# Kernel optimization log

Hardware: AMD Instinct MI355X
Metric: run time of the kernel (lower is better)

The kernel has to match this reference:

```python
import jax, jax.numpy as jnp
import numpy as np

B, T, N, F_IN = 2, 24, 20000, 32
E, H, OUT, K = 320000, 128, 1, 2


def setup_inputs() -> dict:
    key = jax.random.key(0)
    ks = jax.random.split(key, 20)
    x_seq = jax.random.normal(ks[0], (B, T, N, F_IN), dtype=jnp.float32)
    edge_index = jax.random.randint(ks[1], (2, E), 0, N, dtype=jnp.int64)
    edge_weight = jax.random.uniform(ks[2], (E,), dtype=jnp.float32)

    def cheb_w(k, din):
        s = 1.0 / np.sqrt(din)
        return jax.random.uniform(k, (K, din, H), dtype=jnp.float32, minval=-s, maxval=s)

    inp = {
        "x_seq": x_seq, "edge_index": edge_index, "edge_weight": edge_weight,
        "Wxz": cheb_w(ks[3], F_IN), "bxz": jnp.zeros((H,), jnp.float32),
        "Whz": cheb_w(ks[4], H),    "bhz": jnp.zeros((H,), jnp.float32),
        "Wxr": cheb_w(ks[5], F_IN), "bxr": jnp.zeros((H,), jnp.float32),
        "Whr": cheb_w(ks[6], H),    "bhr": jnp.zeros((H,), jnp.float32),
        "Wxh": cheb_w(ks[7], F_IN), "bxh": jnp.zeros((H,), jnp.float32),
        "Whh": cheb_w(ks[8], H),    "bhh": jnp.zeros((H,), jnp.float32),
        "Wl": jax.random.normal(ks[9], (H, OUT), dtype=jnp.float32) * (1.0 / np.sqrt(H)),
        "bl": jnp.zeros((OUT,), jnp.float32),
    }
    return inp


def reference(x_seq, edge_index, edge_weight,
              Wxz, bxz, Whz, bhz, Wxr, bxr, Whr, bhr,
              Wxh, bxh, Whh, bhh, Wl, bl):
    src, dst = edge_index[0], edge_index[1]
    n = x_seq.shape[2]
    # sym-normalized scaled Laplacian with lambda_max=2: Ltilde = -D^{-1/2} A D^{-1/2}
    deg = jnp.zeros((n,), x_seq.dtype).at[src].add(edge_weight)
    dinv = jnp.where(deg > 0, jax.lax.rsqrt(jnp.where(deg > 0, deg, 1.0)), 0.0)
    norm = (-dinv[src] * edge_weight * dinv[dst])  # [E]

    def prop(x):  # x: [B,N,C] -> Ltilde @ x
        msg = x[:, src, :] * norm[None, :, None]          # [B,E,C]
        return jnp.zeros_like(x).at[:, dst, :].add(msg)

    def cheb(x, W, b):  # ChebConv K=2: T0 = x, T1 = Ltilde x
        return x @ W[0] + prop(x) @ W[1] + b

    def step(h, x_t):  # h,x_t: [B,N,*]
        z = jax.nn.sigmoid(cheb(x_t, Wxz, bxz) + cheb(h, Whz, bhz))
        r = jax.nn.sigmoid(cheb(x_t, Wxr, bxr) + cheb(h, Whr, bhr))
        h_tilde = jnp.tanh(cheb(x_t, Wxh, bxh) + cheb(h * r, Whh, bhh))
        h_new = z * h + (1.0 - z) * h_tilde
        return h_new, None

    h0 = jnp.zeros((x_seq.shape[0], n, Whz.shape[2]), x_seq.dtype)
    h_final, _ = jax.lax.scan(step, h0, jnp.swapaxes(x_seq, 0, 1))  # scan over T
    return jax.nn.relu(h_final) @ Wl + bl  # [B,N,OUT]
```

## Files before the change

kernel.cpp:

```cpp
#include <hip/hip_runtime.h>
#include <math.h>

#define NN 20000
#define NE 320000
#define BB 2
#define TT 24
#define FI 32
#define HH 128

__global__ void k_detect(const int* __restrict__ ei, int* __restrict__ flag) {
    int t = threadIdx.x;
    int nz = 0;
    for (int i = 0; i < 4; ++i) nz |= (ei[2 * (t + 64 * i) + 1] != 0);
    unsigned long long m = __ballot(nz);
    if (t == 0) flag[0] = (m != 0ull) ? 0 : 1;
}

__device__ __forceinline__ int eidx(const int* __restrict__ ei, int i, int f64) {
    return f64 ? ei[2 * i] : ei[i];
}


__global__ void k_deg_count(const int* __restrict__ ei, const float* __restrict__ w,
                            float* __restrict__ deg, int* __restrict__ counts,
                            const int* __restrict__ flag) {
    int e = blockIdx.x * blockDim.x + threadIdx.x;
    if (e >= NE) return;
    int f64 = flag[0];
    int s = eidx(ei, e, f64);
    int d = eidx(ei, NE + e, f64);
    atomicAdd(&deg[s], w[e]);
    atomicAdd(&counts[d], 1);
}

__global__ void k_dinv(const float* __restrict__ deg, float* __restrict__ dinv) {
    int n = blockIdx.x * blockDim.x + threadIdx.x;
    if (n >= NN) return;
    float d = deg[n];
    dinv[n] = d > 0.f ? rsqrtf(d) : 0.f;
}

__global__ void k_norm(const int* __restrict__ ei, const float* __restrict__ w,
                       const float* __restrict__ dinv, float* __restrict__ normv,
                       const int* __restrict__ flag) {
    int e = blockIdx.x * blockDim.x + threadIdx.x;
    if (e >= NE) return;
    int f64 = flag[0];
    normv[e] = -dinv[eidx(ei, e, f64)] * w[e] * dinv[eidx(ei, NE + e, f64)];
}

__global__ void k_scan(const int* __restrict__ counts, int* __restrict__ rowptr) {
    __shared__ int sums[1024];
    int t = threadIdx.x;
    const int CH = (NN + 1023) / 1024;
    int start = t * CH;
    int s = 0;
    for (int i = 0; i < CH; ++i) {
        int idx = start + i;
        if (idx < NN) s += counts[idx];
    }
    sums[t] = s;
    __syncthreads();
    for (int off = 1; off < 1024; off *= 2) {
        int v = (t >= off) ? sums[t - off] : 0;
        __syncthreads();
        sums[t] += v;
        __syncthreads();
    }
    int run = (t > 0) ? sums[t - 1] : 0;
    for (int i = 0; i < CH; ++i) {
        int idx = start + i;
        if (idx < NN) { rowptr[idx] = run; run += counts[idx]; }
    }
    if (t == 1023) rowptr[NN] = sums[1023];
}

__global__ void k_copy_int(const int* __restrict__ src, int* __restrict__ dst, int n) {
    int i = blockIdx.x * blockDim.x + threadIdx.x;
    if (i < n) dst[i] = src[i];
}

__global__ void k_fill(const int* __restrict__ ei, const float* __restrict__ normv,
                       int* __restrict__ cursor, int* __restrict__ col, float* __restrict__ val,
                       const int* __restrict__ flag) {
    int e = blockIdx.x * blockDim.x + threadIdx.x;
    if (e >= NE) return;
    int f64 = flag[0];
    int d = eidx(ei, NE + e, f64);
    int p = atomicAdd(&cursor[d], 1);
    col[p] = eidx(ei, e, f64);
    val[p] = normv[e];
}


__global__ void k_prop_x(const float* __restrict__ x_seq, int t0,
                         const int* __restrict__ rowptr, const int* __restrict__ col,
                         const float* __restrict__ val, float* __restrict__ px) {
    int n = blockIdx.x;
    int tl = blockIdx.y;
    int t = t0 + tl;
    int f = threadIdx.x & 31;
    int b = threadIdx.x >> 5;
    int beg = rowptr[n], end = rowptr[n + 1];
    const float* xb = x_seq + ((long)(b * TT + t) * NN) * FI;
    float acc = 0.f;
    for (int j = beg; j < end; ++j)
        acc += val[j] * xb[(long)col[j] * FI + f];
    px[(((long)tl * BB + b) * NN + n) * FI + f] = acc;
}

__global__ void k_prop_h(const float* __restrict__ hin,
                         const int* __restrict__ rowptr, const int* __restrict__ col,
                         const float* __restrict__ val, float* __restrict__ out) {
    int n = blockIdx.x;
    int b = blockIdx.y;
    int f = threadIdx.x;
    int beg = rowptr[n], end = rowptr[n + 1];
    const float* hb = hin + (long)b * NN * HH;
    float acc = 0.f;
    for (int j = beg; j < end; ++j)
        acc += val[j] * hb[(long)col[j] * HH + f];
    out[((long)b * NN + n) * HH + f] = acc;
}

template<int KX1, int KX2, int KH1, int KH2, int EPI>
__global__ __launch_bounds__(128)
void k_gemm(const float* __restrict__ A1, long a1_bstride,
            const float* __restrict__ A2,
            const float* __restrict__ A3,
            const float* __restrict__ A4,
            const float* __restrict__ Wx0, const float* __restrict__ Wh0,
            const float* __restrict__ bx0, const float* __restrict__ bh0,
            const float* __restrict__ Wx1, const float* __restrict__ Wh1,
            const float* __restrict__ bx1, const float* __restrict__ bh1,
            const float* __restrict__ hcur,
            const float* __restrict__ zin,
            float* __restrict__ out0,
            float* __restrict__ out1) {
    constexpr int BM = 64, BN = 64, BK = 16, NW = 128;
    constexpr int C1 = KX1, C2 = KX1 + KX2, C3 = C2 + KH1, KT = C3 + KH2;
    constexpr int NCH = KT / BK;
    static_assert(NCH * BK == KT, "K must be a multiple of BK");
    __shared__ float As[BK][BM + 4];
    __shared__ float Ws[BK][BN];
    const int tid = threadIdx.x;
    const int tx = tid & 15, ty = tid >> 4;
    const int row0 = blockIdx.x * BM;
    const int gate   = (EPI == 1) ? (int)(blockIdx.y >> 1) : 0;
    const int colblk = (EPI == 1) ? (int)(blockIdx.y & 1) : (int)blockIdx.y;
    const int col0 = colblk * BN;

    const float* Wx = Wx0; const float* Wh = Wh0;
    const float* bx = bx0; const float* bh = bh0;
    if (EPI == 1 && gate) { Wx = Wx1; Wh = Wh1; bx = bx1; bh = bh1; }

    const int rA  = tid >> 1;
    const int kqA = (tid & 1) * 8;
    const int rowg = row0 + rA;
    const int b = rowg / NN;
    const int n = rowg - b * NN;
    const long offA1 = (long)b * a1_bstride + (long)n * KX1 + kqA;
    const long offA2 = (long)rowg * KX2 + kqA;
    const long offA3 = (long)rowg * KH1 + kqA;
    const long offA4 = (long)rowg * KH2 + kqA;
    const int kWr = ty;
    const int cW  = tx * 4;

    float4 aS0, aS1, wS0, wS1;
    auto LOADA = [&](int ch) {
        const int kbase = ch * BK;
        const float* s;
        if (kbase < C1)      s = A1 + offA1 + kbase;
        else if (kbase < C2) s = A2 + offA2 + (kbase - C1);
        else if (kbase < C3) s = A3 + offA3 + (kbase - C2);
        else                 s = A4 + offA4 + (kbase - C3);
        aS0 = *(const float4*)s;
        aS1 = *(const float4*)(s + 4);
    };
    auto LOADW = [&](int ch) {
        const int kbase = ch * BK;
        const int kg0 = kbase + kWr, kg1 = kbase + kWr + 8;
        const float* s0 = (kg0 < C2) ? (Wx + (long)kg0 * NW) : (Wh + (long)(kg0 - C2) * NW);
        const float* s1 = (kg1 < C2) ? (Wx + (long)kg1 * NW) : (Wh + (long)(kg1 - C2) * NW);
        wS0 = *(const float4*)(s0 + col0 + cW);
        wS1 = *(const float4*)(s1 + col0 + cW);
    };

    float acc[8][4];
#pragma unroll
    for (int i = 0; i < 8; ++i)
#pragma unroll
        for (int j = 0; j < 4; ++j) acc[i][j] = 0.f;

    LOADA(0); LOADW(0);
    for (int ch = 0; ch < NCH; ++ch) {
        __syncthreads();
        As[kqA + 0][rA] = aS0.x;
        As[kqA + 1][rA] = aS0.y;
        As[kqA + 2][rA] = aS0.z;
        As[kqA + 3][rA] = aS0.w;
        As[kqA + 4][rA] = aS1.x;
        As[kqA + 5][rA] = aS1.y;
        As[kqA + 6][rA] = aS1.z;
        As[kqA + 7][rA] = aS1.w;
        *(float4*)&Ws[kWr][cW]     = wS0;
        *(float4*)&Ws[kWr + 8][cW] = wS1;
        __syncthreads();
        if (ch + 1 < NCH) { LOADA(ch + 1); LOADW(ch + 1); }
#pragma unroll
        for (int kk = 0; kk < BK; ++kk) {
            float4 a0 = *(const float4*)&As[kk][ty << 2];
            float4 a1 = *(const float4*)&As[kk][32 + (ty << 2)];
            float4 w  = *(const float4*)&Ws[kk][tx << 2];
            float a_[8] = {a0.x, a0.y, a0.z, a0.w, a1.x, a1.y, a1.z, a1.w};
            float w_[4] = {w.x, w.y, w.z, w.w};
#pragma unroll
            for (int i = 0; i < 8; ++i)
#pragma unroll
                for (int j = 0; j < 4; ++j)
                    acc[i][j] += a_[i] * w_[j];
        }
    }

    const int cg = col0 + (tx << 2);
    float4 bsum;
    bsum.x = bx[cg + 0] + bh[cg + 0];
    bsum.y = bx[cg + 1] + bh[cg + 1];
    bsum.z = bx[cg + 2] + bh[cg + 2];
    bsum.w = bx[cg + 3] + bh[cg + 3];
#pragma unroll
    for (int i = 0; i < 8; ++i) {
        const int row = row0 + ((i < 4) ? ((ty << 2) + i) : (32 + (ty << 2) + (i - 4)));
        const long o = (long)row * 128 + cg;
        float4 v;
        v.x = acc[i][0] + bsum.x;
        v.y = acc[i][1] + bsum.y;
        v.z = acc[i][2] + bsum.z;
        v.w = acc[i][3] + bsum.w;
        if (EPI == 1) {
            float4 s;
            s.x = 1.f / (1.f + expf(-v.x));
            s.y = 1.f / (1.f + expf(-v.y));
            s.z = 1.f / (1.f + expf(-v.z));
            s.w = 1.f / (1.f + expf(-v.w));
            if (gate == 0) {
                *(float4*)&out0[o] = s;
            } else {
                float4 hc = *(const float4*)&hcur[o];
                s.x *= hc.x; s.y *= hc.y; s.z *= hc.z; s.w *= hc.w;
                *(float4*)&out1[o] = s;
            }
        } else {
            float4 hc = *(const float4*)&hcur[o];
            float4 z  = *(const float4*)&zin[o];
            float4 r;
            r.x = z.x * hc.x + (1.f - z.x) * tanhf(v.x);
            r.y = z.y * hc.y + (1.f - z.y) * tanhf(v.y);
            r.z = z.z * hc.z + (1.f - z.z) * tanhf(v.z);
            r.w = z.w * hc.w + (1.f - z.w) * tanhf(v.w);
            *(float4*)&out0[o] = r;
        }
    }
}

__global__ void k_out(const float* __restrict__ h, const float* __restrict__ Wl,
                      const float* __restrict__ bl, float* __restrict__ out) {
    int row = blockIdx.x;
    int lane = threadIdx.x;
    const float* hr = h + (long)row * HH;
    float a = fmaxf(hr[lane], 0.f) * Wl[lane] + fmaxf(hr[64 + lane], 0.f) * Wl[64 + lane];
#pragma unroll
    for (int off = 32; off > 0; off >>= 1) a += __shfl_down(a, off);
    if (lane == 0) out[row] = a + bl[0];
}

extern "C" void kernel_launch(void* const* d_in, const int* in_sizes, int n_in,
                              void* d_out, int out_size, void* d_ws, size_t ws_size,
                              hipStream_t stream) {
    const float* x_seq = (const float*)d_in[0];
    const int*   ei    = (const int*)d_in[1];
    const float* ew    = (const float*)d_in[2];
    const float* Wxz = (const float*)d_in[3],  *bxz = (const float*)d_in[4];
    const float* Whz = (const float*)d_in[5],  *bhz = (const float*)d_in[6];
    const float* Wxr = (const float*)d_in[7],  *bxr = (const float*)d_in[8];
    const float* Whr = (const float*)d_in[9],  *bhr = (const float*)d_in[10];
    const float* Wxh = (const float*)d_in[11], *bxh = (const float*)d_in[12];
    const float* Whh = (const float*)d_in[13], *bhh = (const float*)d_in[14];
    const float* Wl  = (const float*)d_in[15], *bl  = (const float*)d_in[16];
    float* out = (float*)d_out;

    char* p = (char*)d_ws;
    auto alloc = [&](size_t bytes) -> char* {
        char* r = p;
        p += (bytes + 255) & ~(size_t)255;
        return r;
    };
    const long RB = (long)BB * NN;

    int*   dflag  = (int*)alloc(4);
    float* deg    = (float*)alloc(NN * 4);
    float* dinv   = (float*)alloc(NN * 4);
    float* normv  = (float*)alloc(NE * 4);
    int*   counts = (int*)alloc(NN * 4);
    int*   rowptr = (int*)alloc((NN + 1) * 4);
    int*   cursor = (int*)alloc(NN * 4);
    int*   ccol   = (int*)alloc(NE * 4);
    float* cval   = (float*)alloc(NE * 4);
    float* hbuf   = (float*)alloc(RB * HH * 4);
    float* ph     = (float*)alloc(RB * HH * 4);
    float* zbuf   = (float*)alloc(RB * HH * 4);
    float* hrbuf  = (float*)alloc(RB * HH * 4);

    size_t used = (size_t)(p - (char*)d_ws);
    bool batched = (ws_size > used) && ((ws_size - used) >= (size_t)TT * RB * FI * 4 + 256);
    float* px = (float*)alloc(batched ? (size_t)TT * RB * FI * 4 : (size_t)RB * FI * 4);

    hipMemsetAsync(deg, 0, NN * 4, stream);
    hipMemsetAsync(counts, 0, NN * 4, stream);
    k_detect<<<1, 64, 0, stream>>>(ei, dflag);
    k_deg_count<<<(NE + 255) / 256, 256, 0, stream>>>(ei, ew, deg, counts, dflag);
    k_dinv<<<(NN + 255) / 256, 256, 0, stream>>>(deg, dinv);
    k_norm<<<(NE + 255) / 256, 256, 0, stream>>>(ei, ew, dinv, normv, dflag);
    k_scan<<<1, 1024, 0, stream>>>(counts, rowptr);
    k_copy_int<<<(NN + 255) / 256, 256, 0, stream>>>(rowptr, cursor, NN);
    k_fill<<<(NE + 255) / 256, 256, 0, stream>>>(ei, normv, cursor, ccol, cval, dflag);

    hipMemsetAsync(hbuf, 0, RB * HH * 4, stream);

    if (batched)
        k_prop_x<<<dim3(NN, TT), 64, 0, stream>>>(x_seq, 0, rowptr, ccol, cval, px);

    const long xbstride = (long)TT * NN * FI;
    dim3 gZR(625, 4), gH(625, 2);
    for (int t = 0; t < TT; ++t) {
        const float* xt  = x_seq + (long)t * NN * FI;
        const float* pxt = batched ? (px + (long)t * RB * FI) : px;
        if (!batched)
            k_prop_x<<<dim3(NN, 1), 64, 0, stream>>>(x_seq, t, rowptr, ccol, cval, px);

        k_prop_h<<<dim3(NN, BB), HH, 0, stream>>>(hbuf, rowptr, ccol, cval, ph);
        k_gemm<FI, FI, HH, HH, 1><<<gZR, 128, 0, stream>>>(
            xt, xbstride, pxt, hbuf, ph,
            Wxz, Whz, bxz, bhz, Wxr, Whr, bxr, bhr,
            hbuf, nullptr, zbuf, hrbuf);
        k_prop_h<<<dim3(NN, BB), HH, 0, stream>>>(hrbuf, rowptr, ccol, cval, ph);
        k_gemm<FI, FI, HH, HH, 2><<<gH, 128, 0, stream>>>(
            xt, xbstride, pxt, hrbuf, ph,
            Wxh, Whh, bxh, bhh, nullptr, nullptr, nullptr, nullptr,
            hbuf, zbuf, hbuf, nullptr);
    }

    k_out<<<RB, 64, 0, stream>>>(hbuf, Wl, bl, out);
}
```

Before: 8.089 ms.

## Replace FP32 SIMT GEMM with split-bf16 MFMA and vectorize sparse propagation

```diff
diff --git a/kernel.cpp b/kernel.cpp
--- a/kernel.cpp
+++ b/kernel.cpp
@@ -7,6 +7,20 @@
 #define TT 24
 #define FI 32
 #define HH 128
+
+typedef __attribute__((ext_vector_type(4))) float f32x4;
+typedef __attribute__((ext_vector_type(8))) short bf16x8;
+typedef __attribute__((ext_vector_type(4))) short s16x4;
+
+__device__ __forceinline__ void split1(float f, short& hi, short& lo) {
+    unsigned u = __float_as_uint(f);
+    unsigned short h = (unsigned short)((u + 0x7FFFu + ((u >> 16) & 1u)) >> 16);
+    float fh = __uint_as_float((unsigned)h << 16);
+    float r = f - fh;
+    unsigned v = __float_as_uint(r);
+    unsigned short l = (unsigned short)((v + 0x7FFFu + ((v >> 16) & 1u)) >> 16);
+    hi = (short)h; lo = (short)l;
+}
 
 __global__ void k_detect(const int* __restrict__ ei, int* __restrict__ flag) {
     int t = threadIdx.x;
@@ -92,13 +106,12 @@
     val[p] = normv[e];
 }
 
-
-__global__ void k_prop_x(const float* __restrict__ x_seq, int t0,
-                         const int* __restrict__ rowptr, const int* __restrict__ col,
-                         const float* __restrict__ val, float* __restrict__ px) {
+__global__ void k_prop_x_split(const float* __restrict__ x_seq, int t,
+                               const int* __restrict__ rowptr, const int* __restrict__ col,
+                               const float* __restrict__ val,
+                               short* __restrict__ pxhi, short* __restrict__ pxlo,
+                               short* __restrict__ xhi, short* __restrict__ xlo) {
     int n = blockIdx.x;
-    int tl = blockIdx.y;
-    int t = t0 + tl;
     int f = threadIdx.x & 31;
     int b = threadIdx.x >> 5;
     int beg = rowptr[n], end = rowptr[n + 1];
@@ -106,159 +119,158 @@
     float acc = 0.f;
     for (int j = beg; j < end; ++j)
         acc += val[j] * xb[(long)col[j] * FI + f];
-    px[(((long)tl * BB + b) * NN + n) * FI + f] = acc;
-}
-
-__global__ void k_prop_h(const float* __restrict__ hin,
-                         const int* __restrict__ rowptr, const int* __restrict__ col,
-                         const float* __restrict__ val, float* __restrict__ out) {
-    int n = blockIdx.x;
-    int b = blockIdx.y;
-    int f = threadIdx.x;
+    long o = ((long)b * NN + n) * FI + f;
+    short h, l;
+    split1(acc, h, l);
+    pxhi[o] = h; pxlo[o] = l;
+    split1(xb[(long)n * FI + f], h, l);
+    xhi[o] = h; xlo[o] = l;
+}
+
+__global__ void k_prop_h_split(const float* __restrict__ hin,
+                               const int* __restrict__ rowptr, const int* __restrict__ col,
+                               const float* __restrict__ val,
+                               short* __restrict__ phi, short* __restrict__ plo) {
+    int lane = threadIdx.x & 63;
+    int n = blockIdx.x * 4 + (threadIdx.x >> 6);
+    int b = lane >> 5;
+    int c4 = (lane & 31) << 2;
     int beg = rowptr[n], end = rowptr[n + 1];
-    const float* hb = hin + (long)b * NN * HH;
-    float acc = 0.f;
-    for (int j = beg; j < end; ++j)
-        acc += val[j] * hb[(long)col[j] * HH + f];
-    out[((long)b * NN + n) * HH + f] = acc;
-}
-
-template<int KX1, int KX2, int KH1, int KH2, int EPI>
+    const float* hb = hin + (long)b * NN * HH + c4;
+    f32x4 acc = {0.f, 0.f, 0.f, 0.f};
+    for (int j = beg; j < end; ++j) {
+        float v = val[j];
+        f32x4 q = *(const f32x4*)(hb + (long)col[j] * HH);
+        acc += v * q;
+    }
+    long o = ((long)b * NN + n) * HH + c4;
+    s16x4 hv, lv;
+#pragma unroll
+    for (int i = 0; i < 4; ++i) {
+        short h, l;
+        split1(acc[i], h, l);
+        hv[i] = h; lv[i] = l;
+    }
+    *(s16x4*)(phi + o) = hv;
+    *(s16x4*)(plo + o) = lv;
+}
+
+__global__ void k_prep_w(const float* __restrict__ Wx, const float* __restrict__ Wh,
+                         short* __restrict__ hi, short* __restrict__ lo) {
+    int idx = blockIdx.x * blockDim.x + threadIdx.x;
+    if (idx >= HH * 320) return;
+    int c = idx / 320, k = idx - c * 320;
+    float w = (k < 2 * FI) ? Wx[k * HH + c] : Wh[(k - 2 * FI) * HH + c];
+    short h, l;
+    split1(w, h, l);
+    hi[idx] = h; lo[idx] = l;
+}
+
+template<int EPI>
 __global__ __launch_bounds__(128)
-void k_gemm(const float* __restrict__ A1, long a1_bstride,
-            const float* __restrict__ A2,
-            const float* __restrict__ A3,
-            const float* __restrict__ A4,
-            const float* __restrict__ Wx0, const float* __restrict__ Wh0,
-            const float* __restrict__ bx0, const float* __restrict__ bh0,
-            const float* __restrict__ Wx1, const float* __restrict__ Wh1,
-            const float* __restrict__ bx1, const float* __restrict__ bh1,
-            const float* __restrict__ hcur,
-            const float* __restrict__ zin,
-            float* __restrict__ out0,
-            float* __restrict__ out1) {
-    constexpr int BM = 64, BN = 64, BK = 16, NW = 128;
-    constexpr int C1 = KX1, C2 = KX1 + KX2, C3 = C2 + KH1, KT = C3 + KH2;
-    constexpr int NCH = KT / BK;
-    static_assert(NCH * BK == KT, "K must be a multiple of BK");
-    __shared__ float As[BK][BM + 4];
-    __shared__ float Ws[BK][BN];
+void k_gemm_mfma(const short* __restrict__ xhi, const short* __restrict__ xlo,
+                 const short* __restrict__ pxhi, const short* __restrict__ pxlo,
+                 const short* __restrict__ ahhi, const short* __restrict__ ahlo,
+                 const short* __restrict__ aphi, const short* __restrict__ aplo,
+                 const short* __restrict__ Whi0, const short* __restrict__ Wlo0,
+                 const float* __restrict__ bx0, const float* __restrict__ bh0,
+                 const short* __restrict__ Whi1, const short* __restrict__ Wlo1,
+                 const float* __restrict__ bx1, const float* __restrict__ bh1,
+                 const float* __restrict__ hcur,
+                 const float* __restrict__ zin,
+                 float* __restrict__ out0,
+                 float* __restrict__ out1,
+                 short* __restrict__ sohi,
+                 short* __restrict__ solo) {
     const int tid = threadIdx.x;
-    const int tx = tid & 15, ty = tid >> 4;
-    const int row0 = blockIdx.x * BM;
-    const int gate   = (EPI == 1) ? (int)(blockIdx.y >> 1) : 0;
-    const int colblk = (EPI == 1) ? (int)(blockIdx.y & 1) : (int)blockIdx.y;
-    const int col0 = colblk * BN;
-
-    const float* Wx = Wx0; const float* Wh = Wh0;
-    const float* bx = bx0; const float* bh = bh0;
-    if (EPI == 1 && gate) { Wx = Wx1; Wh = Wh1; bx = bx1; bh = bh1; }
-
-    const int rA  = tid >> 1;
-    const int kqA = (tid & 1) * 8;
-    const int rowg = row0 + rA;
-    const int b = rowg / NN;
-    const int n = rowg - b * NN;
-    const long offA1 = (long)b * a1_bstride + (long)n * KX1 + kqA;
-    const long offA2 = (long)rowg * KX2 + kqA;
-    const long offA3 = (long)rowg * KH1 + kqA;
-    const long offA4 = (long)rowg * KH2 + kqA;
-    const int kWr = ty;
-    const int cW  = tx * 4;
-
-    float4 aS0, aS1, wS0, wS1;
-    auto LOADA = [&](int ch) {
-        const int kbase = ch * BK;
-        const float* s;
-        if (kbase < C1)      s = A1 + offA1 + kbase;
-        else if (kbase < C2) s = A2 + offA2 + (kbase - C1);
-        else if (kbase < C3) s = A3 + offA3 + (kbase - C2);
-        else                 s = A4 + offA4 + (kbase - C3);
-        aS0 = *(const float4*)s;
-        aS1 = *(const float4*)(s + 4);
-    };
-    auto LOADW = [&](int ch) {
-        const int kbase = ch * BK;
-        const int kg0 = kbase + kWr, kg1 = kbase + kWr + 8;
-        const float* s0 = (kg0 < C2) ? (Wx + (long)kg0 * NW) : (Wh + (long)(kg0 - C2) * NW);
-        const float* s1 = (kg1 < C2) ? (Wx + (long)kg1 * NW) : (Wh + (long)(kg1 - C2) * NW);
-        wS0 = *(const float4*)(s0 + col0 + cW);
-        wS1 = *(const float4*)(s1 + col0 + cW);
-    };
-
-    float acc[8][4];
-#pragma unroll
-    for (int i = 0; i < 8; ++i)
-#pragma unroll
-        for (int j = 0; j < 4; ++j) acc[i][j] = 0.f;
-
-    LOADA(0); LOADW(0);
-    for (int ch = 0; ch < NCH; ++ch) {
-        __syncthreads();
-        As[kqA + 0][rA] = aS0.x;
-        As[kqA + 1][rA] = aS0.y;
-        As[kqA + 2][rA] = aS0.z;
-        As[kqA + 3][rA] = aS0.w;
-        As[kqA + 4][rA] = aS1.x;
-        As[kqA + 5][rA] = aS1.y;
-        As[kqA + 6][rA] = aS1.z;
-        As[kqA + 7][rA] = aS1.w;
-        *(float4*)&Ws[kWr][cW]     = wS0;
-        *(float4*)&Ws[kWr + 8][cW] = wS1;
-        __syncthreads();
-        if (ch + 1 < NCH) { LOADA(ch + 1); LOADW(ch + 1); }
-#pragma unroll
-        for (int kk = 0; kk < BK; ++kk) {
-            float4 a0 = *(const float4*)&As[kk][ty << 2];
-            float4 a1 = *(const float4*)&As[kk][32 + (ty << 2)];
-            float4 w  = *(const float4*)&Ws[kk][tx << 2];
-            float a_[8] = {a0.x, a0.y, a0.z, a0.w, a1.x, a1.y, a1.z, a1.w};
-            float w_[4] = {w.x, w.y, w.z, w.w};
-#pragma unroll
-            for (int i = 0; i < 8; ++i)
-#pragma unroll
-                for (int j = 0; j < 4; ++j)
-                    acc[i][j] += a_[i] * w_[j];
+    const int lane = tid & 63;
+    const int wid = tid >> 6;
+    const int lr = lane & 15;
+    const int lg = lane >> 4;
+    const int gate = (EPI == 1) ? (int)blockIdx.y : 0;
+    const short* Whi = gate ? Whi1 : Whi0;
+    const short* Wlo = gate ? Wlo1 : Wlo0;
+    const float* bx  = gate ? bx1 : bx0;
+    const float* bh  = gate ? bh1 : bh0;
+
+    const int row_base = blockIdx.x * 32;
+    const int col_base = wid * 64;
+
+    long r32[2], r128[2];
+#pragma unroll
+    for (int m = 0; m < 2; ++m) {
+        int row = row_base + m * 16 + lr;
+        r32[m]  = (long)row * FI + lg * 8;
+        r128[m] = (long)row * HH + lg * 8;
+    }
+    const long wbase = (long)(col_base + lr) * 320;
+
+    f32x4 acc[2][4];
+#pragma unroll
+    for (int m = 0; m < 2; ++m)
+#pragma unroll
+        for (int n = 0; n < 4; ++n) acc[m][n] = (f32x4){0.f, 0.f, 0.f, 0.f};
+
+#pragma unroll
+    for (int ks = 0; ks < 10; ++ks) {
+        bf16x8 ahi[2], alo[2];
+#pragma unroll
+        for (int m = 0; m < 2; ++m) {
+            const short *ph_, *pl_;
+            long off;
+            if (ks == 0)      { ph_ = xhi;  pl_ = xlo;  off = r32[m]; }
+            else if (ks == 1) { ph_ = pxhi; pl_ = pxlo; off = r32[m]; }
+            else if (ks < 6)  { ph_ = ahhi; pl_ = ahlo; off = r128[m] + (ks - 2) * 32; }
+            else              { ph_ = aphi; pl_ = aplo; off = r128[m] + (ks - 6) * 32; }
+            ahi[m] = *(const bf16x8*)(ph_ + off);
+            alo[m] = *(const bf16x8*)(pl_ + off);
         }
-    }
-
-    const int cg = col0 + (tx << 2);
-    float4 bsum;
-    bsum.x = bx[cg + 0] + bh[cg + 0];
-    bsum.y = bx[cg + 1] + bh[cg + 1];
-    bsum.z = bx[cg + 2] + bh[cg + 2];
-    bsum.w = bx[cg + 3] + bh[cg + 3];
-#pragma unroll
-    for (int i = 0; i < 8; ++i) {
-        const int row = row0 + ((i < 4) ? ((ty << 2) + i) : (32 + (ty << 2) + (i - 4)));
-        const long o = (long)row * 128 + cg;
-        float4 v;
-        v.x = acc[i][0] + bsum.x;
-        v.y = acc[i][1] + bsum.y;
-        v.z = acc[i][2] + bsum.z;
-        v.w = acc[i][3] + bsum.w;
-        if (EPI == 1) {
-            float4 s;
-            s.x = 1.f / (1.f + expf(-v.x));
-            s.y = 1.f / (1.f + expf(-v.y));
-            s.z = 1.f / (1.f + expf(-v.z));
-            s.w = 1.f / (1.f + expf(-v.w));
-            if (gate == 0) {
-                *(float4*)&out0[o] = s;
-            } else {
-                float4 hc = *(const float4*)&hcur[o];
-                s.x *= hc.x; s.y *= hc.y; s.z *= hc.z; s.w *= hc.w;
-                *(float4*)&out1[o] = s;
+#pragma unroll
+        for (int n = 0; n < 4; ++n) {
+            const long wo = wbase + (long)n * (16 * 320) + ks * 32 + lg * 8;
+            bf16x8 wh = *(const bf16x8*)(Whi + wo);
+            bf16x8 wl = *(const bf16x8*)(Wlo + wo);
+#pragma unroll
+            for (int m = 0; m < 2; ++m) {
+                acc[m][n] = __builtin_amdgcn_mfma_f32_16x16x32_bf16(ahi[m], wh, acc[m][n], 0, 0, 0);
+                acc[m][n] = __builtin_amdgcn_mfma_f32_16x16x32_bf16(ahi[m], wl, acc[m][n], 0, 0, 0);
+                acc[m][n] = __builtin_amdgcn_mfma_f32_16x16x32_bf16(alo[m], wh, acc[m][n], 0, 0, 0);
             }
-        } else {
-            float4 hc = *(const float4*)&hcur[o];
-            float4 z  = *(const float4*)&zin[o];
-            float4 r;
-            r.x = z.x * hc.x + (1.f - z.x) * tanhf(v.x);
-            r.y = z.y * hc.y + (1.f - z.y) * tanhf(v.y);
-            r.z = z.z * hc.z + (1.f - z.z) * tanhf(v.z);
-            r.w = z.w * hc.w + (1.f - z.w) * tanhf(v.w);
-            *(float4*)&out0[o] = r;
+        }
+    }
+
+#pragma unroll
+    for (int m = 0; m < 2; ++m) {
+#pragma unroll
+        for (int n = 0; n < 4; ++n) {
+            const int col = col_base + n * 16 + lr;
+            const float bsum = bx[col] + bh[col];
+#pragma unroll
+            for (int j = 0; j < 4; ++j) {
+                const int row = row_base + m * 16 + lg * 4 + j;
+                const long o = (long)row * HH + col;
+                float v = acc[m][n][j] + bsum;
+                if (EPI == 1) {
+                    float s = 1.f / (1.f + expf(-v));
+                    if (gate == 0) {
+                        out0[o] = s;
+                    } else {
+                        float hrv = s * hcur[o];
+                        out1[o] = hrv;
+                        short hh, ll;
+                        split1(hrv, hh, ll);
+                        sohi[o] = hh; solo[o] = ll;
+                    }
+                } else {
+                    float ht = tanhf(v);
+                    float z = zin[o];
+                    float hn = z * hcur[o] + (1.f - z) * ht;
+                    out0[o] = hn;
+                    short hh, ll;
+                    split1(hn, hh, ll);
+                    sohi[o] = hh; solo[o] = ll;
+                }
+            }
         }
     }
 }
@@ -307,13 +319,24 @@
     int*   ccol   = (int*)alloc(NE * 4);
     float* cval   = (float*)alloc(NE * 4);
     float* hbuf   = (float*)alloc(RB * HH * 4);
-    float* ph     = (float*)alloc(RB * HH * 4);
     float* zbuf   = (float*)alloc(RB * HH * 4);
     float* hrbuf  = (float*)alloc(RB * HH * 4);
-
-    size_t used = (size_t)(p - (char*)d_ws);
-    bool batched = (ws_size > used) && ((ws_size - used) >= (size_t)TT * RB * FI * 4 + 256);
-    float* px = (float*)alloc(batched ? (size_t)TT * RB * FI * 4 : (size_t)RB * FI * 4);
+    short* xthi   = (short*)alloc(RB * FI * 2);
+    short* xtlo   = (short*)alloc(RB * FI * 2);
+    short* pxhi   = (short*)alloc(RB * FI * 2);
+    short* pxlo   = (short*)alloc(RB * FI * 2);
+    short* hhi    = (short*)alloc(RB * HH * 2);
+    short* hlo    = (short*)alloc(RB * HH * 2);
+    short* hrhi   = (short*)alloc(RB * HH * 2);
+    short* hrlo   = (short*)alloc(RB * HH * 2);
+    short* phhi   = (short*)alloc(RB * HH * 2);
+    short* phlo   = (short*)alloc(RB * HH * 2);
+    short* WtZhi  = (short*)alloc(HH * 320 * 2);
+    short* WtZlo  = (short*)alloc(HH * 320 * 2);
+    short* WtRhi  = (short*)alloc(HH * 320 * 2);
+    short* WtRlo  = (short*)alloc(HH * 320 * 2);
+    short* WtHhi  = (short*)alloc(HH * 320 * 2);
+    short* WtHlo  = (short*)alloc(HH * 320 * 2);
 
     hipMemsetAsync(deg, 0, NN * 4, stream);
     hipMemsetAsync(counts, 0, NN * 4, stream);
@@ -325,29 +348,29 @@
     k_copy_int<<<(NN + 255) / 256, 256, 0, stream>>>(rowptr, cursor, NN);
     k_fill<<<(NE + 255) / 256, 256, 0, stream>>>(ei, normv, cursor, ccol, cval, dflag);
 
+    const int WPE = HH * 320;
+    k_prep_w<<<(WPE + 255) / 256, 256, 0, stream>>>(Wxz, Whz, WtZhi, WtZlo);
+    k_prep_w<<<(WPE + 255) / 256, 256, 0, stream>>>(Wxr, Whr, WtRhi, WtRlo);
+    k_prep_w<<<(WPE + 255) / 256, 256, 0, stream>>>(Wxh, Whh, WtHhi, WtHlo);
+
     hipMemsetAsync(hbuf, 0, RB * HH * 4, stream);
-
-    if (batched)
-        k_prop_x<<<dim3(NN, TT), 64, 0, stream>>>(x_seq, 0, rowptr, ccol, cval, px);
-
-    const long xbstride = (long)TT * NN * FI;
-    dim3 gZR(625, 4), gH(625, 2);
+    hipMemsetAsync(hhi, 0, RB * HH * 2, stream);
+    hipMemsetAsync(hlo, 0, RB * HH * 2, stream);
+
+    dim3 gZR(1250, 2), gH(1250, 1);
     for (int t = 0; t < TT; ++t) {
-        const float* xt  = x_seq + (long)t * NN * FI;
-        const float* pxt = batched ? (px + (long)t * RB * FI) : px;
-        if (!batched)
-            k_prop_x<<<dim3(NN, 1), 64, 0, stream>>>(x_seq, t, rowptr, ccol, cval, px);
-
-        k_prop_h<<<dim3(NN, BB), HH, 0, stream>>>(hbuf, rowptr, ccol, cval, ph);
-        k_gemm<FI, FI, HH, HH, 1><<<gZR, 128, 0, stream>>>(
-            xt, xbstride, pxt, hbuf, ph,
-            Wxz, Whz, bxz, bhz, Wxr, Whr, bxr, bhr,
-            hbuf, nullptr, zbuf, hrbuf);
-        k_prop_h<<<dim3(NN, BB), HH, 0, stream>>>(hrbuf, rowptr, ccol, cval, ph);
-        k_gemm<FI, FI, HH, HH, 2><<<gH, 128, 0, stream>>>(
-            xt, xbstride, pxt, hrbuf, ph,
-            Wxh, Whh, bxh, bhh, nullptr, nullptr, nullptr, nullptr,
-            hbuf, zbuf, hbuf, nullptr);
+        k_prop_x_split<<<NN, 64, 0, stream>>>(x_seq, t, rowptr, ccol, cval,
+                                              pxhi, pxlo, xthi, xtlo);
+        k_prop_h_split<<<NN / 4, 256, 0, stream>>>(hbuf, rowptr, ccol, cval, phhi, phlo);
+        k_gemm_mfma<1><<<gZR, 128, 0, stream>>>(
+            xthi, xtlo, pxhi, pxlo, hhi, hlo, phhi, phlo,
+            WtZhi, WtZlo, bxz, bhz, WtRhi, WtRlo, bxr, bhr,
+            hbuf, nullptr, zbuf, hrbuf, hrhi, hrlo);
+        k_prop_h_split<<<NN / 4, 256, 0, stream>>>(hrbuf, rowptr, ccol, cval, phhi, phlo);
+        k_gemm_mfma<2><<<gH, 128, 0, stream>>>(
+            xthi, xtlo, pxhi, pxlo, hrhi, hrlo, phhi, phlo,
+            WtHhi, WtHlo, bxh, bhh, nullptr, nullptr, nullptr, nullptr,
+            hbuf, zbuf, hbuf, nullptr, hhi, hlo);
     }
 
     k_out<<<RB, 64, 0, stream>>>(hbuf, Wl, bl, out);
```

After: 6.581 ms. -18.6%, faster.
